# Kernel tuning notes

Hardware: AMD Instinct MI355X
Metric: run time of the kernel (lower is better)

## Reference

```python
import jax, jax.numpy as jnp
import numpy as np

N, E, B, D, L = 100000, 600000, 128, 128, 3
BOT = 64
EPS = 1e-5


def _forward(query_x, corpus_x, gin_eps, mlp_W1, mlp_b1, mlp_W2, mlp_b2, bn_gamma, bn_beta,
             pool_G1, pool_g1b, pool_G2, pool_g2b, pool_Wm,
             int_G1, int_g1b, int_G2, int_g2b, int_F1, int_f1b, int_F2, int_f2b,
             sc_G1, sc_g1b, sc_G2, sc_g2b, sc_F1, sc_f1b, sc_F2, sc_f2b,
             query_edge_index, query_graph_idx, corpus_edge_index, corpus_graph_idx, num_graphs):
    def gin(x, ei, l):
        # GINConv: sum of source-node features into targets, plus (1+eps)*self
        agg = jax.ops.segment_sum(x[ei[0]], ei[1], num_segments=x.shape[0])
        h = (1.0 + gin_eps[l]) * x + agg
        h = jax.nn.relu(h @ mlp_W1[l] + mlp_b1[l]) @ mlp_W2[l] + mlp_b2[l]
        mu = h.mean(axis=0)
        var = ((h - mu) ** 2).mean(axis=0)  # biased var (BatchNorm training mode)
        h = (h - mu) * jax.lax.rsqrt(var + EPS) * bn_gamma[l] + bn_beta[l]
        return jax.nn.relu(h)  # dropout p=0.0

    def pool(x, gidx, l):
        coef = jnp.tanh(jax.nn.relu(x @ pool_G1[l] + pool_g1b[l]) @ pool_G2[l] + pool_g2b[l])
        s = (coef + 1.0) * x
        sums = jax.ops.segment_sum(s, gidx, num_segments=num_graphs)
        cnt = jax.ops.segment_sum(jnp.ones((x.shape[0],), x.dtype), gidx, num_segments=num_graphs)
        mean = sums / cnt[:, None]
        gc = jnp.tanh(mean @ pool_Wm[l])  # [B, D]
        node_coef = jax.nn.sigmoid(jnp.sum(s * gc[gidx], axis=1))  # [N]
        return jax.ops.segment_sum(node_coef[:, None] * s, gidx, num_segments=num_graphs)

    def interact(q, c, l):
        comb = jnp.concatenate([q, c], axis=1)  # [B, 2D]
        coef = jax.nn.sigmoid(jax.nn.relu(comb @ int_G1[l] + int_g1b[l]) @ int_G2[l] + int_g2b[l])
        sc = (coef + 1.0) * comb
        return jax.nn.relu(jax.nn.relu(sc @ int_F1[l] + int_f1b[l]) @ int_F2[l] + int_f2b[l])

    qx, cx = query_x, corpus_x
    feats = []
    for l in range(gin_eps.shape[0]):
        qx = gin(qx, query_edge_index, l)
        cx = gin(cx, corpus_edge_index, l)
        feats.append(interact(pool(qx, query_graph_idx, l), pool(cx, corpus_graph_idx, l), l))
    f = jnp.concatenate(feats, axis=1)  # [B, sum(filters)//2]
    coef = jax.nn.sigmoid(jax.nn.relu(f @ sc_G1 + sc_g1b) @ sc_G2 + sc_g2b)
    sf = (coef + 1.0) * f
    return (jax.nn.relu(sf @ sc_F1 + sc_f1b) @ sc_F2 + sc_f2b).squeeze(-1)  # [B]


def setup_inputs() -> dict:
    key = jax.random.key(0)
    kit = iter(jax.random.split(key, 64))
    def nrm(shape, s=0.05):
        return jax.random.normal(next(kit), shape, jnp.float32) * s
    C, R, OUT, AGG, RG = 2 * D, (2 * D) // 4, D // 2, (3 * D) // 2, ((3 * D) // 2) // 4
    inp = {
        "query_x": nrm((N, D), 1.0),
        "query_edge_index": jax.random.randint(next(kit), (2, E), 0, N),
        "query_graph_idx": jnp.sort(jax.random.randint(next(kit), (N,), 0, B)),
        "corpus_x": nrm((N, D), 1.0),
        "corpus_edge_index": jax.random.randint(next(kit), (2, E), 0, N),
        "corpus_graph_idx": jnp.sort(jax.random.randint(next(kit), (N,), 0, B)),
        "num_graphs": B,
        "gin_eps": jnp.zeros((L,), jnp.float32),
        "mlp_W1": nrm((L, D, D)), "mlp_b1": jnp.zeros((L, D)),
        "mlp_W2": nrm((L, D, D)), "mlp_b2": jnp.zeros((L, D)),
        "bn_gamma": jnp.ones((L, D)), "bn_beta": jnp.zeros((L, D)),
        "pool_G1": nrm((L, D, D // 4)), "pool_g1b": jnp.zeros((L, D // 4)),
        "pool_G2": nrm((L, D // 4, D)), "pool_g2b": jnp.zeros((L, D)),
        "pool_Wm": nrm((L, D, D)),
        "int_G1": nrm((L, C, R)), "int_g1b": jnp.zeros((L, R)),
        "int_G2": nrm((L, R, C)), "int_g2b": jnp.zeros((L, C)),
        "int_F1": nrm((L, C, C)), "int_f1b": jnp.zeros((L, C)),
        "int_F2": nrm((L, C, OUT)), "int_f2b": jnp.zeros((L, OUT)),
        "sc_G1": nrm((AGG, RG)), "sc_g1b": jnp.zeros((RG,)),
        "sc_G2": nrm((RG, AGG)), "sc_g2b": jnp.zeros((AGG,)),
        "sc_F1": nrm((AGG, BOT)), "sc_f1b": jnp.zeros((BOT,)),
        "sc_F2": nrm((BOT, 1)), "sc_f2b": jnp.zeros((1,)),
    }
    return inp


def reference(query_x, query_edge_index, query_graph_idx, corpus_x, corpus_edge_index, corpus_graph_idx,
              num_graphs, gin_eps, mlp_W1, mlp_b1, mlp_W2, mlp_b2, bn_gamma, bn_beta,
              pool_G1, pool_g1b, pool_G2, pool_g2b, pool_Wm,
              int_G1, int_g1b, int_G2, int_g2b, int_F1, int_f1b, int_F2, int_f2b,
              sc_G1, sc_g1b, sc_G2, sc_g2b, sc_F1, sc_f1b, sc_F2, sc_f2b):
    return _forward(query_x, corpus_x, gin_eps, mlp_W1, mlp_b1, mlp_W2, mlp_b2, bn_gamma, bn_beta,
                    pool_G1, pool_g1b, pool_G2, pool_g2b, pool_Wm,
                    int_G1, int_g1b, int_G2, int_g2b, int_F1, int_f1b, int_F2, int_f2b,
                    sc_G1, sc_g1b, sc_G2, sc_g2b, sc_F1, sc_f1b, sc_F2, sc_f2b,
                    query_edge_index, query_graph_idx, corpus_edge_index, corpus_graph_idx, num_graphs)
```

## Files before the change

### kernel.cpp

```cpp
#include <hip/hip_runtime.h>
#include <hip/hip_bf16.h>

constexpr int NN  = 100000;
constexpr int NN2 = 200000;
constexpr int NE  = 600000;
constexpr int NB  = 128;
constexpr int D   = 128;
constexpr int NL  = 3;
constexpr int CAP = 48;
constexpr int MT_TOT = NN2 / 16;
constexpr int MT_Q   = NN / 16;

constexpr int PREP_CSR   = (2 * NE + 255) / 256;
constexpr int PREP_WPREP = 1956;
constexpr int PREP_CNT   = 64;
constexpr int PREP_TOT   = PREP_CSR + PREP_WPREP + PREP_CNT;

constexpr int NCSEG_BLK = 1024;

typedef __bf16 bf16x8 __attribute__((ext_vector_type(8)));
typedef float f32x4 __attribute__((ext_vector_type(4)));
typedef unsigned short us8 __attribute__((ext_vector_type(8)));

__device__ __forceinline__ float sigmoidf_(float x) { return 1.0f / (1.0f + __expf(-x)); }
__device__ __forceinline__ unsigned short f2b(float f) {
    __hip_bfloat16 h = __float2bfloat16(f);
    return __builtin_bit_cast(unsigned short, h);
}
__device__ __forceinline__ float b2f(unsigned short u) {
    __hip_bfloat16 h = __builtin_bit_cast(__hip_bfloat16, u);
    return __bfloat162float(h);
}
__device__ __forceinline__ bf16x8 ldfrag(const unsigned short* p) {
    return __builtin_bit_cast(bf16x8, *(const us8*)p);
}

__device__ __forceinline__ void ncseg_body(int vbid, int nstream_blocks,
                                           const unsigned short* __restrict__ S,
                                           const int* __restrict__ gq, const int* __restrict__ gc,
                                           const float* __restrict__ gcb,
                                           float* __restrict__ dq, float* __restrict__ dc) {
    int stream = vbid * 4 + (threadIdx.x >> 6);
    int lane = threadIdx.x & 63;
    int nstream = nstream_blocks * 4;
    int per = (NN2 + nstream - 1) / nstream;
    int r0 = stream * per;
    int r1 = min(r0 + per, NN2);
    if (r0 >= r1) return;
    float a0 = 0.f, a1 = 0.f;
    int cur = (r0 < NN) ? gq[r0] : 128 + gc[r0 - NN];
    for (int r = r0; r < r1; ++r) {
        int g = (r < NN) ? gq[r] : 128 + gc[r - NN];
        if (g != cur) {
            float* base = (cur < 128) ? (dq + cur * D) : (dc + (cur - 128) * D);
            atomicAdd(&base[lane * 2], a0);
            atomicAdd(&base[lane * 2 + 1], a1);
            a0 = 0.f; a1 = 0.f; cur = g;
        }
        ushort2 sv = *(const ushort2*)&S[(size_t)r * D + lane * 2];
        float2 gv = *(const float2*)&gcb[(size_t)g * D + lane * 2];
        float v0 = b2f(sv.x), v1 = b2f(sv.y);
        float p = v0 * gv.x + v1 * gv.y;
#pragma unroll
        for (int off = 1; off < 64; off <<= 1) p += __shfl_xor(p, off, 64);
        float nc = sigmoidf_(p);
        a0 += nc * v0; a1 += nc * v1;
    }
    float* base = (cur < 128) ? (dq + cur * D) : (dc + (cur - 128) * D);
    atomicAdd(&base[lane * 2], a0);
    atomicAdd(&base[lane * 2 + 1], a1);
}

__device__ __forceinline__ void gather_bf16_body(int vbid,
                                                 const unsigned short* __restrict__ xb,
                                                 unsigned short* __restrict__ z,
                                                 const int* __restrict__ deg, const int* __restrict__ bucket,
                                                 float e) {
    int r = vbid * 16 + (threadIdx.x >> 4);
    int c8 = threadIdx.x & 15;
    float a[8];
    us8 v = *(const us8*)(xb + (size_t)r * D + c8 * 8);
#pragma unroll
    for (int j = 0; j < 8; ++j) a[j] = e * b2f(v[j]);
    int d = deg[r]; d = (d < CAP) ? d : CAP;
    const int* bk = bucket + (size_t)r * CAP;
    int i = 0;
    for (; i + 4 <= d; i += 4) {
        int s0 = bk[i], s1 = bk[i + 1], s2 = bk[i + 2], s3 = bk[i + 3];
        us8 u0 = *(const us8*)(xb + (size_t)s0 * D + c8 * 8);
        us8 u1 = *(const us8*)(xb + (size_t)s1 * D + c8 * 8);
        us8 u2 = *(const us8*)(xb + (size_t)s2 * D + c8 * 8);
        us8 u3 = *(const us8*)(xb + (size_t)s3 * D + c8 * 8);
#pragma unroll
        for (int j = 0; j < 8; ++j)
            a[j] += b2f(u0[j]) + b2f(u1[j]) + b2f(u2[j]) + b2f(u3[j]);
    }
    for (; i < d; ++i) {
        int s0 = bk[i];
        us8 u0 = *(const us8*)(xb + (size_t)s0 * D + c8 * 8);
#pragma unroll
        for (int j = 0; j < 8; ++j) a[j] += b2f(u0[j]);
    }
    us8 o;
#pragma unroll
    for (int j = 0; j < 8; ++j) o[j] = f2b(a[j]);
    *(us8*)(z + (size_t)r * D + c8 * 8) = o;
}

__global__ __launch_bounds__(256) void k_prep(
    const int* __restrict__ qei, const int* __restrict__ cei,
    int* __restrict__ deg, int* __restrict__ bucket,
    const float* mW1, const float* mW2, const float* pG1, const float* pG2,
    const float* iG1, const float* iG2, const float* iF1, const float* iF2,
    const float* sG1, const float* sG2, const float* sF1,
    unsigned short* W1t, unsigned short* W2t, unsigned short* G1t, unsigned short* G2t,
    unsigned short* iG1t, unsigned short* iG2t, unsigned short* iF1t, unsigned short* iF2t,
    unsigned short* sG1t, unsigned short* sG2t, unsigned short* sF1t,
    const int* __restrict__ gq, const int* __restrict__ gc, float* __restrict__ cnt) {
    if (blockIdx.x < PREP_CSR) {
        int e = blockIdx.x * 256 + threadIdx.x;
        int src, dst;
        if (e < NE) {
            src = qei[e]; dst = qei[NE + e];
        } else if (e < 2 * NE) {
            src = cei[e - NE] + NN; dst = cei[NE + (e - NE)] + NN;
        } else return;
        int pos = atomicAdd(&deg[dst], 1);
        if (pos < CAP) bucket[(size_t)dst * CAP + pos] = src;
        return;
    }
    if (blockIdx.x < PREP_CSR + PREP_WPREP) {
        int i = (blockIdx.x - PREP_CSR) * 256 + threadIdx.x;
#define SEG(CNT, KK, NN_, SRC, DST)                                              \
        if (i < (CNT)) {                                                         \
            int l = i / ((KK) * (NN_)), r = i % ((KK) * (NN_));                  \
            int n = r / (KK), k = r % (KK);                                      \
            DST[i] = f2b(SRC[(size_t)l * (KK) * (NN_) + (size_t)k * (NN_) + n]); \
            return;                                                              \
        }                                                                        \
        i -= (CNT);
        SEG(49152, 128, 128, mW1, W1t)
        SEG(49152, 128, 128, mW2, W2t)
        SEG(12288, 128, 32, pG1, G1t)
        SEG(12288, 32, 128, pG2, G2t)
        SEG(49152, 256, 64, iG1, iG1t)
        SEG(49152, 64, 256, iG2, iG2t)
        SEG(196608, 256, 256, iF1, iF1t)
        SEG(49152, 256, 64, iF2, iF2t)
        SEG(9216, 192, 48, sG1, sG1t)
        if (i < 12288) {
            int n = i / 64, k = i % 64;
            sG2t[i] = (k < 48) ? f2b(sG2[(size_t)k * 192 + n]) : (unsigned short)0;
            return;
        }
        i -= 12288;
        SEG(12288, 192, 64, sF1, sF1t)
#undef SEG
        return;
    }
    {
        __shared__ float h[256];
        int vb = blockIdx.x - (PREP_CSR + PREP_WPREP);
        for (int i = threadIdx.x; i < 256; i += 256) h[i] = 0.f;
        __syncthreads();
        int total = PREP_CNT * 256;
        int tid = vb * 256 + threadIdx.x;
        int per = (NN2 + total - 1) / total;
        int r0 = tid * per, r1 = min(r0 + per, NN2);
        if (r0 < r1) {
            int cur = (r0 < NN) ? gq[r0] : 128 + gc[r0 - NN];
            float c = 0.f;
            for (int r = r0; r < r1; ++r) {
                int g = (r < NN) ? gq[r] : 128 + gc[r - NN];
                if (g != cur) { atomicAdd(&h[cur], c); c = 0.f; cur = g; }
                c += 1.f;
            }
            atomicAdd(&h[cur], c);
        }
        __syncthreads();
        for (int i = threadIdx.x; i < 256; i += 256)
            if (h[i] != 0.f) atomicAdd(&cnt[i], h[i]);
    }
}

__global__ __launch_bounds__(256) void k_gather0(const float* __restrict__ qx, const float* __restrict__ cx,
                                                 unsigned short* __restrict__ z,
                                                 const int* __restrict__ deg, const int* __restrict__ bucket,
                                                 const float* __restrict__ eps_p) {
    int r = blockIdx.x * 16 + (threadIdx.x >> 4);
    int c8 = threadIdx.x & 15;
    float e = 1.0f + eps_p[0];
    float a[8];
    const float* base = (r < NN) ? qx : cx;
    int off = (r < NN) ? 0 : NN;
    float4 v0 = *(const float4*)(base + (size_t)(r - off) * D + c8 * 8);
    float4 v1 = *(const float4*)(base + (size_t)(r - off) * D + c8 * 8 + 4);
    a[0] = e * v0.x; a[1] = e * v0.y; a[2] = e * v0.z; a[3] = e * v0.w;
    a[4] = e * v1.x; a[5] = e * v1.y; a[6] = e * v1.z; a[7] = e * v1.w;
    int d = deg[r]; d = (d < CAP) ? d : CAP;
    const int* bk = bucket + (size_t)r * CAP;
    int i = 0;
    for (; i + 4 <= d; i += 4) {
        int s0 = bk[i], s1 = bk[i + 1], s2 = bk[i + 2], s3 = bk[i + 3];
        const float* p0 = base + (size_t)(s0 - off) * D + c8 * 8;
        const float* p1 = base + (size_t)(s1 - off) * D + c8 * 8;
        const float* p2 = base + (size_t)(s2 - off) * D + c8 * 8;
        const float* p3 = base + (size_t)(s3 - off) * D + c8 * 8;
        float4 w0 = *(const float4*)p0, w0b = *(const float4*)(p0 + 4);
        float4 w1 = *(const float4*)p1, w1b = *(const float4*)(p1 + 4);
        float4 w2 = *(const float4*)p2, w2b = *(const float4*)(p2 + 4);
        float4 w3 = *(const float4*)p3, w3b = *(const float4*)(p3 + 4);
        a[0] += w0.x + w1.x + w2.x + w3.x; a[1] += w0.y + w1.y + w2.y + w3.y;
        a[2] += w0.z + w1.z + w2.z + w3.z; a[3] += w0.w + w1.w + w2.w + w3.w;
        a[4] += w0b.x + w1b.x + w2b.x + w3b.x; a[5] += w0b.y + w1b.y + w2b.y + w3b.y;
        a[6] += w0b.z + w1b.z + w2b.z + w3b.z; a[7] += w0b.w + w1b.w + w2b.w + w3b.w;
    }
    for (; i < d; ++i) {
        int s0 = bk[i];
        const float* p0 = base + (size_t)(s0 - off) * D + c8 * 8;
        float4 w0 = *(const float4*)p0, w0b = *(const float4*)(p0 + 4);
        a[0] += w0.x; a[1] += w0.y; a[2] += w0.z; a[3] += w0.w;
        a[4] += w0b.x; a[5] += w0b.y; a[6] += w0b.z; a[7] += w0b.w;
    }
    us8 o;
#pragma unroll
    for (int j = 0; j < 8; ++j) o[j] = f2b(a[j]);
    *(us8*)(z + (size_t)r * D + c8 * 8) = o;
}

__global__ __launch_bounds__(256) void k_gncseg(const unsigned short* __restrict__ xb,
                                                unsigned short* __restrict__ z,
                                                const int* __restrict__ deg, const int* __restrict__ bucket,
                                                const float* __restrict__ eps_p, int l,
                                                const unsigned short* __restrict__ S,
                                                const int* __restrict__ gq, const int* __restrict__ gcix,
                                                const float* __restrict__ gcb,
                                                float* __restrict__ dq, float* __restrict__ dc) {
    if (blockIdx.x < NCSEG_BLK) {
        ncseg_body(blockIdx.x, NCSEG_BLK, S, gq, gcix, gcb, dq, dc);
    } else {
        float e = 1.0f + eps_p[l];
        gather_bf16_body(blockIdx.x - NCSEG_BLK, xb, z, deg, bucket, e);
    }
}

__global__ __launch_bounds__(256) void k_ncseg(const unsigned short* __restrict__ S,
                                               const int* __restrict__ gq, const int* __restrict__ gc,
                                               const float* __restrict__ gcb,
                                               float* __restrict__ dq, float* __restrict__ dc) {
    ncseg_body(blockIdx.x, NCSEG_BLK, S, gq, gc, gcb, dq, dc);
}

constexpr int HSTR = 136;
__global__ __launch_bounds__(256, 2) void k_mlp(unsigned short* zh,
                                                const unsigned short* __restrict__ W1t,
                                                const unsigned short* __restrict__ W2t,
                                                const float* __restrict__ b1,
                                                const float* __restrict__ b2,
                                                float* __restrict__ stat) {
    __shared__ unsigned short hb[2][2][16 * HSTR];
    __shared__ float red[512];
    int wave = threadIdx.x >> 6, lane = threadIdx.x & 63;
    int col16 = lane & 15, quad = lane >> 4;
    int g = wave >> 1, half = wave & 1;
    bf16x8 bf1[4][4], bf2[4][4];
    float bb1[4], bb2[4];
#pragma unroll
    for (int t = 0; t < 4; ++t) {
        int c = half * 64 + t * 16 + col16;
        bb1[t] = b1[c]; bb2[t] = b2[c];
#pragma unroll
        for (int kc = 0; kc < 4; ++kc) {
            bf1[t][kc] = ldfrag(W1t + (size_t)c * D + kc * 32 + quad * 8);
            bf2[t][kc] = ldfrag(W2t + (size_t)c * D + kc * 32 + quad * 8);
        }
    }
    float cs[2][4] = {{0.f,0.f,0.f,0.f},{0.f,0.f,0.f,0.f}};
    float cq[2][4] = {{0.f,0.f,0.f,0.f},{0.f,0.f,0.f,0.f}};
    int groups = gridDim.x * 2;
    int iters = (MT_TOT + groups - 1) / groups;
    for (int n = 0; n < iters; ++n) {
        int mt = blockIdx.x * 2 + g + n * groups;
        bool act = (mt < MT_TOT);
        int pp = n & 1;
        unsigned short* hbuf = hb[pp][g];
        {
            const unsigned short* Ap = zh + ((size_t)(act ? mt : 0) * 16 + col16) * D + quad * 8;
            f32x4 acc[4];
#pragma unroll
            for (int t = 0; t < 4; ++t) acc[t] = (f32x4){0.f, 0.f, 0.f, 0.f};
#pragma unroll
            for (int kc = 0; kc < 4; ++kc) {
                bf16x8 af = ldfrag(Ap + kc * 32);
#pragma unroll
                for (int t = 0; t < 4; ++t)
                    acc[t] = __builtin_amdgcn_mfma_f32_16x16x32_bf16(af, bf1[t][kc], acc[t], 0, 0, 0);
            }
#pragma unroll
            for (int t = 0; t < 4; ++t) {
                int c = half * 64 + t * 16 + col16;
#pragma unroll
                for (int r = 0; r < 4; ++r)
                    hbuf[(quad * 4 + r) * HSTR + c] = f2b(fmaxf(acc[t][r] + bb1[t], 0.f));
            }
        }
        __syncthreads();
        {
            f32x4 acc[4];
#pragma unroll
            for (int t = 0; t < 4; ++t) acc[t] = (f32x4){0.f, 0.f, 0.f, 0.f};
#pragma unroll
            for (int kc = 0; kc < 4; ++kc) {
                bf16x8 af = ldfrag(&hbuf[col16 * HSTR + kc * 32 + quad * 8]);
#pragma unroll
                for (int t = 0; t < 4; ++t)
                    acc[t] = __builtin_amdgcn_mfma_f32_16x16x32_bf16(af, bf2[t][kc], acc[t], 0, 0, 0);
            }
            if (act) {
                int side = (mt < MT_Q) ? 0 : 1;
#pragma unroll
                for (int t = 0; t < 4; ++t) {
                    int c = half * 64 + t * 16 + col16;
#pragma unroll
                    for (int r = 0; r < 4; ++r) {
                        int m = mt * 16 + quad * 4 + r;
                        float v = acc[t][r] + bb2[t];
                        zh[(size_t)m * D + c] = f2b(v);
                        cs[side][t] += v; cq[side][t] += v * v;
                    }
                }
            }
        }
    }
    for (int i = threadIdx.x; i < 512; i += 256) red[i] = 0.f;
    __syncthreads();
#pragma unroll
    for (int t = 0; t < 4; ++t) {
        int c = half * 64 + t * 16 + col16;
#pragma unroll
        for (int side = 0; side < 2; ++side) {
            atomicAdd(&red[side * 256 + c], cs[side][t]);
            atomicAdd(&red[side * 256 + 128 + c], cq[side][t]);
        }
    }
    __syncthreads();
    for (int i = threadIdx.x; i < 512; i += 256) atomicAdd(&stat[i], red[i]);
}

__global__ __launch_bounds__(256, 2) void k_pool(const unsigned short* __restrict__ H,
                                                 const unsigned short* __restrict__ G1t,
                                                 const unsigned short* __restrict__ G2t,
                                                 const float* __restrict__ b1,
                                                 const float* __restrict__ b2,
                                                 const float* __restrict__ stat,
                                                 const float* __restrict__ gamma,
                                                 const float* __restrict__ beta,
                                                 const int* __restrict__ gq, const int* __restrict__ gcix,
                                                 unsigned short* __restrict__ Xo,
                                                 unsigned short* __restrict__ S,
                                                 float* __restrict__ seg_sum) {
    __shared__ float sc_s[256], sh_s[256];
    __shared__ unsigned short xt[4][16 * HSTR];
    __shared__ unsigned short t2t[4][16 * 40];
    {
        int t = threadIdx.x, side = t >> 7, c = t & 127;
        const float invN = 1.0f / (float)NN;
        float mu = stat[side * 256 + c] * invN;
        float var = fmaxf(stat[side * 256 + 128 + c] * invN - mu * mu, 0.f);
        float inv = rsqrtf(var + 1e-5f);
        float s = gamma[c] * inv;
        sc_s[t] = s;
        sh_s[t] = beta[c] - mu * s;
    }
    __syncthreads();
    int wave = threadIdx.x >> 6, lane = threadIdx.x & 63;
    int col16 = lane & 15, quad = lane >> 4;
    unsigned short* xtile = xt[wave];
    unsigned short* t2tile = t2t[wave];
    int nwaves = gridDim.x * 4;
    int per = (MT_TOT + nwaves - 1) / nwaves;
    int wid = blockIdx.x * 4 + wave;
    int mt0 = wid * per, mt1 = min(mt0 + per, MT_TOT);
    if (mt0 >= mt1) return;

    bf16x8 g1f[2][4], g2f[8];
    float bb1[2], bb2[8];
#pragma unroll
    for (int t = 0; t < 2; ++t) {
        int c = t * 16 + col16;
        bb1[t] = b1[c];
#pragma unroll
        for (int kc = 0; kc < 4; ++kc)
            g1f[t][kc] = ldfrag(G1t + (size_t)c * D + kc * 32 + quad * 8);
    }
#pragma unroll
    for (int t = 0; t < 8; ++t) {
        int c = t * 16 + col16;
        bb2[t] = b2[c];
        g2f[t] = ldfrag(G2t + (size_t)c * 32 + quad * 8);
    }
    float sacc[8] = {0.f, 0.f, 0.f, 0.f, 0.f, 0.f, 0.f, 0.f};
    int curg = -1;
    for (int mt = mt0; mt < mt1; ++mt) {
        int side = (mt < MT_Q) ? 0 : 1;
        const float* scp = sc_s + side * 128;
        const float* shp = sh_s + side * 128;
        const unsigned short* Hp = H + ((size_t)mt * 16 + col16) * D + quad * 8;
        unsigned short* Xp = Xo + ((size_t)mt * 16 + col16) * D + quad * 8;
        f32x4 acc1[2];
#pragma unroll
        for (int t = 0; t < 2; ++t) acc1[t] = (f32x4){0.f, 0.f, 0.f, 0.f};
#pragma unroll
        for (int kc = 0; kc < 4; ++kc) {
            us8 hv = *(const us8*)(Hp + kc * 32);
            int k0 = kc * 32 + quad * 8;
            float4 s0 = *(const float4*)&scp[k0], s1 = *(const float4*)&scp[k0 + 4];
            float4 h0 = *(const float4*)&shp[k0], h1 = *(const float4*)&shp[k0 + 4];
            us8 xv;
            xv[0] = f2b(fmaxf(b2f(hv[0]) * s0.x + h0.x, 0.f));
            xv[1] = f2b(fmaxf(b2f(hv[1]) * s0.y + h0.y, 0.f));
            xv[2] = f2b(fmaxf(b2f(hv[2]) * s0.z + h0.z, 0.f));
            xv[3] = f2b(fmaxf(b2f(hv[3]) * s0.w + h0.w, 0.f));
            xv[4] = f2b(fmaxf(b2f(hv[4]) * s1.x + h1.x, 0.f));
            xv[5] = f2b(fmaxf(b2f(hv[5]) * s1.y + h1.y, 0.f));
            xv[6] = f2b(fmaxf(b2f(hv[6]) * s1.z + h1.z, 0.f));
            xv[7] = f2b(fmaxf(b2f(hv[7]) * s1.w + h1.w, 0.f));
            *(us8*)(Xp + kc * 32) = xv;
            *(us8*)(xtile + col16 * HSTR + k0) = xv;
            bf16x8 af = __builtin_bit_cast(bf16x8, xv);
#pragma unroll
            for (int t = 0; t < 2; ++t)
                acc1[t] = __builtin_amdgcn_mfma_f32_16x16x32_bf16(af, g1f[t][kc], acc1[t], 0, 0, 0);
        }
#pragma unroll
        for (int t = 0; t < 2; ++t) {
            int c = t * 16 + col16;
#pragma unroll
            for (int r = 0; r < 4; ++r)
                t2tile[(quad * 4 + r) * 40 + c] = f2b(fmaxf(acc1[t][r] + bb1[t], 0.f));
        }
        bf16x8 af2 = ldfrag(t2tile + col16 * 40 + quad * 8);
        f32x4 acc2[8];
#pragma unroll
        for (int t = 0; t < 8; ++t) {
            acc2[t] = (f32x4){0.f, 0.f, 0.f, 0.f};
            acc2[t] = __builtin_amdgcn_mfma_f32_16x16x32_bf16(af2, g2f[t], acc2[t], 0, 0, 0);
        }
#pragma unroll
        for (int r = 0; r < 4; ++r) {
            int m = mt * 16 + quad * 4 + r;
            int g = (m < NN) ? gq[m] : 128 + gcix[m - NN];
            if (g != curg) {
                if (curg >= 0) {
#pragma unroll
                    for (int t = 0; t < 8; ++t) {
                        atomicAdd(&seg_sum[(size_t)curg * D + t * 16 + col16], sacc[t]);
                        sacc[t] = 0.f;
                    }
                }
                curg = g;
            }
#pragma unroll
            for (int t = 0; t < 8; ++t) {
                int c = t * 16 + col16;
                float v = (tanhf(acc2[t][r] + bb2[t]) + 1.f) * b2f(xtile[(quad * 4 + r) * HSTR + c]);
                S[(size_t)m * D + c] = f2b(v);
                sacc[t] += v;
            }
        }
    }
    if (curg >= 0) {
#pragma unroll
        for (int t = 0; t < 8; ++t)
            atomicAdd(&seg_sum[(size_t)curg * D + t * 16 + col16], sacc[t]);
    }
}

__global__ void k_gc(float* __restrict__ sums, const float* __restrict__ cnt,
                     const float* __restrict__ Wm, float* __restrict__ gc) {
    __shared__ float m[D];
    int b = blockIdx.x, j = threadIdx.x;
    m[j] = sums[b * D + j] / cnt[b];
    sums[b * D + j] = 0.f;
    __syncthreads();
    float a = 0.f;
#pragma unroll 8
    for (int i = 0; i < D; ++i) a += m[i] * Wm[i * D + j];
    gc[b * D + j] = tanhf(a);
}

constexpr int LSTR = 264;
__global__ __launch_bounds__(256) void k_interact(const float* __restrict__ pooled,
                                                  const unsigned short* __restrict__ iG1t, const float* __restrict__ ig1b,
                                                  const unsigned short* __restrict__ iG2t, const float* __restrict__ ig2b,
                                                  const unsigned short* __restrict__ iF1t, const float* __restrict__ if1b,
                                                  const unsigned short* __restrict__ iF2t, const float* __restrict__ if2b,
                                                  unsigned short* __restrict__ featsb) {
    __shared__ unsigned short bufC[16 * LSTR];
    __shared__ unsigned short bufA[16 * LSTR];
    __shared__ unsigned short bufB[16 * LSTR];
    int t = threadIdx.x, wave = t >> 6, lane = t & 63;
    int col16 = lane & 15, quad = lane >> 4;
    int pg = blockIdx.x & 7, l = blockIdx.x >> 3;
    int p0 = pg * 16;
    {
        int r = t >> 4, c0 = (t & 15) * 16;
        const float* src = (c0 < 128)
            ? (pooled + (size_t)l * NB * D + (size_t)(p0 + r) * D + c0)
            : (pooled + (size_t)(NL + l) * NB * D + (size_t)(p0 + r) * D + (c0 - 128));
#pragma unroll
        for (int j = 0; j < 16; ++j) bufC[r * LSTR + c0 + j] = f2b(src[j]);
    }
    __syncthreads();
    {
        f32x4 acc = (f32x4){0.f, 0.f, 0.f, 0.f};
        int n = wave * 16 + col16;
#pragma unroll
        for (int kc = 0; kc < 8; ++kc) {
            bf16x8 af = ldfrag(&bufC[col16 * LSTR + kc * 32 + quad * 8]);
            bf16x8 bfr = ldfrag(iG1t + ((size_t)l * 64 + n) * 256 + kc * 32 + quad * 8);
            acc = __builtin_amdgcn_mfma_f32_16x16x32_bf16(af, bfr, acc, 0, 0, 0);
        }
        float bb = ig1b[(size_t)l * 64 + n];
#pragma unroll
        for (int r = 0; r < 4; ++r)
            bufA[(quad * 4 + r) * LSTR + n] = f2b(fmaxf(acc[r] + bb, 0.f));
    }
    __syncthreads();
    {
        f32x4 acc[4];
#pragma unroll
        for (int tt = 0; tt < 4; ++tt) acc[tt] = (f32x4){0.f, 0.f, 0.f, 0.f};
#pragma unroll
        for (int kc = 0; kc < 2; ++kc) {
            bf16x8 af = ldfrag(&bufA[col16 * LSTR + kc * 32 + quad * 8]);
#pragma unroll
            for (int tt = 0; tt < 4; ++tt) {
                int n = wave * 64 + tt * 16 + col16;
                bf16x8 bfr = ldfrag(iG2t + ((size_t)l * 256 + n) * 64 + kc * 32 + quad * 8);
                acc[tt] = __builtin_amdgcn_mfma_f32_16x16x32_bf16(af, bfr, acc[tt], 0, 0, 0);
            }
        }
#pragma unroll
        for (int tt = 0; tt < 4; ++tt) {
            int n = wave * 64 + tt * 16 + col16;
            float bb = ig2b[(size_t)l * 256 + n];
#pragma unroll
            for (int r = 0; r < 4; ++r) {
                int row = quad * 4 + r;
                float s = (sigmoidf_(acc[tt][r] + bb) + 1.f) * b2f(bufC[row * LSTR + n]);
                bufB[row * LSTR + n] = f2b(s);
            }
        }
    }
    __syncthreads();
    {
        f32x4 acc[4];
#pragma unroll
        for (int tt = 0; tt < 4; ++tt) acc[tt] = (f32x4){0.f, 0.f, 0.f, 0.f};
#pragma unroll
        for (int kc = 0; kc < 8; ++kc) {
            bf16x8 af = ldfrag(&bufB[col16 * LSTR + kc * 32 + quad * 8]);
#pragma unroll
            for (int tt = 0; tt < 4; ++tt) {
                int n = wave * 64 + tt * 16 + col16;
                bf16x8 bfr = ldfrag(iF1t + (size_t)l * 256 * 256 + (size_t)n * 256 + kc * 32 + quad * 8);
                acc[tt] = __builtin_amdgcn_mfma_f32_16x16x32_bf16(af, bfr, acc[tt], 0, 0, 0);
            }
        }
#pragma unroll
        for (int tt = 0; tt < 4; ++tt) {
            int n = wave * 64 + tt * 16 + col16;
            float bb = if1b[(size_t)l * 256 + n];
#pragma unroll
            for (int r = 0; r < 4; ++r)
                bufA[(quad * 4 + r) * LSTR + n] = f2b(fmaxf(acc[tt][r] + bb, 0.f));
        }
    }
    __syncthreads();
    {
        f32x4 acc = (f32x4){0.f, 0.f, 0.f, 0.f};
        int n = wave * 16 + col16;
#pragma unroll
        for (int kc = 0; kc < 8; ++kc) {
            bf16x8 af = ldfrag(&bufA[col16 * LSTR + kc * 32 + quad * 8]);
            bf16x8 bfr = ldfrag(iF2t + ((size_t)l * 64 + n) * 256 + kc * 32 + quad * 8);
            acc = __builtin_amdgcn_mfma_f32_16x16x32_bf16(af, bfr, acc, 0, 0, 0);
        }
        float bb = if2b[(size_t)l * 64 + n];
#pragma unroll
        for (int r = 0; r < 4; ++r)
            featsb[(size_t)(p0 + quad * 4 + r) * 192 + l * 64 + n] = f2b(fmaxf(acc[r] + bb, 0.f));
    }
}

__global__ __launch_bounds__(256) void k_score(const unsigned short* __restrict__ featsb,
                                               const unsigned short* __restrict__ sG1t, const float* __restrict__ sg1b,
                                               const unsigned short* __restrict__ sG2t, const float* __restrict__ sg2b,
                                               const unsigned short* __restrict__ sF1t, const float* __restrict__ sf1b,
                                               const float* __restrict__ sF2, const float* __restrict__ sf2b,
                                               float* __restrict__ out) {
    __shared__ unsigned short bufF[16 * 200];
    __shared__ unsigned short bufA[16 * LSTR];
    __shared__ unsigned short bufB[16 * LSTR];
    __shared__ float redf[16 * 65];
    int t = threadIdx.x, wave = t >> 6, lane = t & 63;
    int col16 = lane & 15, quad = lane >> 4;
    int p0 = blockIdx.x * 16;
    {
        int r = t >> 4, c0 = (t & 15) * 12;
#pragma unroll
        for (int j = 0; j < 12; ++j)
            bufF[r * 200 + c0 + j] = featsb[(size_t)(p0 + r) * 192 + c0 + j];
    }
    __syncthreads();
    if (wave < 3) {
        f32x4 acc = (f32x4){0.f, 0.f, 0.f, 0.f};
        int n = wave * 16 + col16;
#pragma unroll
        for (int kc = 0; kc < 6; ++kc) {
            bf16x8 af = ldfrag(&bufF[col16 * 200 + kc * 32 + quad * 8]);
            bf16x8 bfr = ldfrag(sG1t + (size_t)n * 192 + kc * 32 + quad * 8);
            acc = __builtin_amdgcn_mfma_f32_16x16x32_bf16(af, bfr, acc, 0, 0, 0);
        }
        float bb = sg1b[n];
#pragma unroll
        for (int r = 0; r < 4; ++r)
            bufA[(quad * 4 + r) * LSTR + n] = f2b(fmaxf(acc[r] + bb, 0.f));
    } else {
        int row = lane >> 2, c = 48 + (lane & 3) * 4;
#pragma unroll
        for (int j = 0; j < 4; ++j) bufA[row * LSTR + c + j] = 0;
    }
    __syncthreads();
    {
        f32x4 acc[3];
#pragma unroll
        for (int tt = 0; tt < 3; ++tt) acc[tt] = (f32x4){0.f, 0.f, 0.f, 0.f};
#pragma unroll
        for (int kc = 0; kc < 2; ++kc) {
            bf16x8 af = ldfrag(&bufA[col16 * LSTR + kc * 32 + quad * 8]);
#pragma unroll
            for (int tt = 0; tt < 3; ++tt) {
                int n = wave * 48 + tt * 16 + col16;
                bf16x8 bfr = ldfrag(sG2t + (size_t)n * 64 + kc * 32 + quad * 8);
                acc[tt] = __builtin_amdgcn_mfma_f32_16x16x32_bf16(af, bfr, acc[tt], 0, 0, 0);
            }
        }
#pragma unroll
        for (int tt = 0; tt < 3; ++tt) {
            int n = wave * 48 + tt * 16 + col16;
            float bb = sg2b[n];
#pragma unroll
            for (int r = 0; r < 4; ++r) {
                int row = quad * 4 + r;
                float s = (sigmoidf_(acc[tt][r] + bb) + 1.f) * b2f(bufF[row * 200 + n]);
                bufB[row * LSTR + n] = f2b(s);
            }
        }
    }
    __syncthreads();
    {
        f32x4 acc = (f32x4){0.f, 0.f, 0.f, 0.f};
        int n = wave * 16 + col16;
#pragma unroll
        for (int kc = 0; kc < 6; ++kc) {
            bf16x8 af = ldfrag(&bufB[col16 * LSTR + kc * 32 + quad * 8]);
            bf16x8 bfr = ldfrag(sF1t + (size_t)n * 192 + kc * 32 + quad * 8);
            acc = __builtin_amdgcn_mfma_f32_16x16x32_bf16(af, bfr, acc, 0, 0, 0);
        }
        float bb = sf1b[n], w2 = sF2[n];
#pragma unroll
        for (int r = 0; r < 4; ++r)
            redf[(quad * 4 + r) * 65 + n] = fmaxf(acc[r] + bb, 0.f) * w2;
    }
    __syncthreads();
    if (t < 16) {
        float s = 0.f;
#pragma unroll 8
        for (int i = 0; i < 64; ++i) s += redf[t * 65 + i];
        out[p0 + t] = s + sf2b[0];
    }
}

extern "C" void kernel_launch(void* const* d_in, const int* in_sizes, int n_in,
                              void* d_out, int out_size, void* d_ws, size_t ws_size,
                              hipStream_t stream) {
    const float* query_x   = (const float*)d_in[0];
    const int*   query_ei  = (const int*)d_in[1];
    const int*   query_gi  = (const int*)d_in[2];
    const float* corpus_x  = (const float*)d_in[3];
    const int*   corpus_ei = (const int*)d_in[4];
    const int*   corpus_gi = (const int*)d_in[5];
    const float* gin_eps   = (const float*)d_in[7];
    const float* mlp_W1    = (const float*)d_in[8];
    const float* mlp_b1    = (const float*)d_in[9];
    const float* mlp_W2    = (const float*)d_in[10];
    const float* mlp_b2    = (const float*)d_in[11];
    const float* bn_gamma  = (const float*)d_in[12];
    const float* bn_beta   = (const float*)d_in[13];
    const float* pool_G1   = (const float*)d_in[14];
    const float* pool_g1b  = (const float*)d_in[15];
    const float* pool_G2   = (const float*)d_in[16];
    const float* pool_g2b  = (const float*)d_in[17];
    const float* pool_Wm   = (const float*)d_in[18];
    const float* int_G1    = (const float*)d_in[19];
    const float* int_g1b   = (const float*)d_in[20];
    const float* int_G2    = (const float*)d_in[21];
    const float* int_g2b   = (const float*)d_in[22];
    const float* int_F1    = (const float*)d_in[23];
    const float* int_f1b   = (const float*)d_in[24];
    const float* int_F2    = (const float*)d_in[25];
    const float* int_f2b   = (const float*)d_in[26];
    const float* sc_G1     = (const float*)d_in[27];
    const float* sc_g1b    = (const float*)d_in[28];
    const float* sc_G2     = (const float*)d_in[29];
    const float* sc_g2b    = (const float*)d_in[30];
    const float* sc_F1     = (const float*)d_in[31];
    const float* sc_f1b    = (const float*)d_in[32];
    const float* sc_F2     = (const float*)d_in[33];
    const float* sc_f2b    = (const float*)d_in[34];
    float* out = (float*)d_out;

    unsigned short* Zb  = (unsigned short*)d_ws;
    unsigned short* Xb  = Zb + (size_t)NN2 * D;
    unsigned short* Sb  = Xb + (size_t)NN2 * D;
    unsigned short* featsb = Sb + (size_t)NN2 * D;
    unsigned short* W1t = featsb + 128 * 192;
    unsigned short* W2t = W1t + NL * D * D;
    unsigned short* G1t = W2t + NL * D * D;
    unsigned short* G2t = G1t + NL * 32 * D;
    unsigned short* iG1t = G2t + NL * D * 32;
    unsigned short* iG2t = iG1t + NL * 64 * 256;
    unsigned short* iF1t = iG2t + NL * 256 * 64;
    unsigned short* iF2t = iF1t + NL * 256 * 256;
    unsigned short* sG1t = iF2t + NL * 64 * 256;
    unsigned short* sG2t = sG1t + 48 * 192;
    unsigned short* sF1t = sG2t + 192 * 64;
    int* deg    = (int*)(sF1t + 64 * 192);
    int* bucket = deg + NN2;
    float* bn_stat  = (float*)(bucket + (size_t)NN2 * CAP);
    float* seg_sum  = bn_stat + NL * 512;
    float* seg_cnt  = seg_sum + 256 * D;
    float* gcb      = seg_cnt + 256;
    float* pooled   = gcb + 256 * D;

    hipMemsetAsync(deg, 0, NN2 * sizeof(int), stream);
    hipMemsetAsync(bn_stat, 0, NL * 512 * sizeof(float), stream);
    hipMemsetAsync(pooled, 0, 2 * NL * NB * D * sizeof(float), stream);
    hipMemsetAsync(seg_cnt, 0, 256 * sizeof(float), stream);
    hipMemsetAsync(seg_sum, 0, 256 * D * sizeof(float), stream);

    k_prep<<<PREP_TOT, 256, 0, stream>>>(query_ei, corpus_ei, deg, bucket,
                                         mlp_W1, mlp_W2, pool_G1, pool_G2,
                                         int_G1, int_G2, int_F1, int_F2,
                                         sc_G1, sc_G2, sc_F1,
                                         W1t, W2t, G1t, G2t, iG1t, iG2t, iF1t, iF2t,
                                         sG1t, sG2t, sF1t,
                                         query_gi, corpus_gi, seg_cnt);

    for (int l = 0; l < NL; ++l) {
        if (l == 0)
            k_gather0<<<MT_TOT, 256, 0, stream>>>(query_x, corpus_x, Zb, deg, bucket, gin_eps);
        else
            k_gncseg<<<NCSEG_BLK + MT_TOT, 256, 0, stream>>>(
                Xb, Zb, deg, bucket, gin_eps, l,
                Sb, query_gi, corpus_gi, gcb,
                pooled + (size_t)(l - 1) * NB * D,
                pooled + (size_t)(NL + l - 1) * NB * D);
        k_mlp<<<1024, 256, 0, stream>>>(Zb, W1t + (size_t)l * D * D, W2t + (size_t)l * D * D,
                                        mlp_b1 + l * D, mlp_b2 + l * D, bn_stat + l * 512);
        k_pool<<<782, 256, 0, stream>>>(Zb, G1t + (size_t)l * 32 * D, G2t + (size_t)l * D * 32,
                                        pool_g1b + l * 32, pool_g2b + l * D,
                                        bn_stat + l * 512, bn_gamma + l * D, bn_beta + l * D,
                                        query_gi, corpus_gi, Xb, Sb, seg_sum);
        k_gc<<<256, D, 0, stream>>>(seg_sum, seg_cnt, pool_Wm + (size_t)l * D * D, gcb);
    }
    k_ncseg<<<NCSEG_BLK, 256, 0, stream>>>(Sb, query_gi, corpus_gi, gcb,
                                           pooled + (size_t)(NL - 1) * NB * D,
                                           pooled + (size_t)(2 * NL - 1) * NB * D);
    k_interact<<<24, 256, 0, stream>>>(pooled, iG1t, int_g1b, iG2t, int_g2b,
                                       iF1t, int_f1b, iF2t, int_f2b, featsb);
    k_score<<<8, 256, 0, stream>>>(featsb, sG1t, sc_g1b, sG2t, sc_g2b,
                                   sF1t, sc_f1b, sc_F2, sc_f2b, out);
}
```

Measured before the change: 998.4 us.

## Restructure MLP kernel to one 32-row tile per block, stream weights from cache

The MLP kernel moves from a persistent grid, where each wave kept its 64-column weight slice in registers, to one block per 32-row tile. Each wave computes 32 columns for both 16-row halves and reloads the W1/W2 fragments from global memory or cache. The block reduces BatchNorm statistics in LDS and adds them to global memory once per block. In the pool kernel, the G1/G2 weight fragments are likewise loaded per tile instead of kept in registers, and the occupancy hints go up (4 and 3 blocks per CU). The goal is to cut register pressure and raise occupancy, in exchange for repeated weight loads and many more global atomics on the stats.

After: 1.227 ms. 22.9% more time.

```diff
diff --git a/kernel.cpp b/kernel.cpp
--- a/kernel.cpp
+++ b/kernel.cpp
@@ -10,6 +10,7 @@
 constexpr int CAP = 48;
 constexpr int MT_TOT = NN2 / 16;
 constexpr int MT_Q   = NN / 16;
+constexpr int ST_TOT = NN2 / 32;
 
 constexpr int PREP_CSR   = (2 * NE + 255) / 256;
 constexpr int PREP_WPREP = 1956;
@@ -252,102 +253,91 @@
 }
 
 constexpr int HSTR = 136;
-__global__ __launch_bounds__(256, 2) void k_mlp(unsigned short* zh,
+__global__ __launch_bounds__(256, 4) void k_mlp(unsigned short* zh,
                                                 const unsigned short* __restrict__ W1t,
                                                 const unsigned short* __restrict__ W2t,
                                                 const float* __restrict__ b1,
                                                 const float* __restrict__ b2,
                                                 float* __restrict__ stat) {
-    __shared__ unsigned short hb[2][2][16 * HSTR];
-    __shared__ float red[512];
-    int wave = threadIdx.x >> 6, lane = threadIdx.x & 63;
+    __shared__ unsigned short hbuf[32 * HSTR];
+    __shared__ float red[256];
+    int tid = threadIdx.x;
+    int wave = tid >> 6, lane = tid & 63;
     int col16 = lane & 15, quad = lane >> 4;
-    int g = wave >> 1, half = wave & 1;
-    bf16x8 bf1[4][4], bf2[4][4];
-    float bb1[4], bb2[4];
-#pragma unroll
-    for (int t = 0; t < 4; ++t) {
-        int c = half * 64 + t * 16 + col16;
-        bb1[t] = b1[c]; bb2[t] = b2[c];
+    int base = blockIdx.x * 32;
+    red[tid] = 0.f;
+    {
+        f32x4 acc[2][2];
+#pragma unroll
+        for (int rt = 0; rt < 2; ++rt)
+#pragma unroll
+            for (int ct = 0; ct < 2; ++ct) acc[rt][ct] = (f32x4){0.f, 0.f, 0.f, 0.f};
 #pragma unroll
         for (int kc = 0; kc < 4; ++kc) {
-            bf1[t][kc] = ldfrag(W1t + (size_t)c * D + kc * 32 + quad * 8);
-            bf2[t][kc] = ldfrag(W2t + (size_t)c * D + kc * 32 + quad * 8);
-        }
-    }
-    float cs[2][4] = {{0.f,0.f,0.f,0.f},{0.f,0.f,0.f,0.f}};
-    float cq[2][4] = {{0.f,0.f,0.f,0.f},{0.f,0.f,0.f,0.f}};
-    int groups = gridDim.x * 2;
-    int iters = (MT_TOT + groups - 1) / groups;
-    for (int n = 0; n < iters; ++n) {
-        int mt = blockIdx.x * 2 + g + n * groups;
-        bool act = (mt < MT_TOT);
-        int pp = n & 1;
-        unsigned short* hbuf = hb[pp][g];
-        {
-            const unsigned short* Ap = zh + ((size_t)(act ? mt : 0) * 16 + col16) * D + quad * 8;
-            f32x4 acc[4];
-#pragma unroll
-            for (int t = 0; t < 4; ++t) acc[t] = (f32x4){0.f, 0.f, 0.f, 0.f};
-#pragma unroll
-            for (int kc = 0; kc < 4; ++kc) {
-                bf16x8 af = ldfrag(Ap + kc * 32);
-#pragma unroll
-                for (int t = 0; t < 4; ++t)
-                    acc[t] = __builtin_amdgcn_mfma_f32_16x16x32_bf16(af, bf1[t][kc], acc[t], 0, 0, 0);
-            }
-#pragma unroll
-            for (int t = 0; t < 4; ++t) {
-                int c = half * 64 + t * 16 + col16;
+            bf16x8 af0 = ldfrag(zh + (size_t)(base + col16) * D + kc * 32 + quad * 8);
+            bf16x8 af1 = ldfrag(zh + (size_t)(base + 16 + col16) * D + kc * 32 + quad * 8);
+#pragma unroll
+            for (int ct = 0; ct < 2; ++ct) {
+                int c = wave * 32 + ct * 16 + col16;
+                bf16x8 wf = ldfrag(W1t + (size_t)c * D + kc * 32 + quad * 8);
+                acc[0][ct] = __builtin_amdgcn_mfma_f32_16x16x32_bf16(af0, wf, acc[0][ct], 0, 0, 0);
+                acc[1][ct] = __builtin_amdgcn_mfma_f32_16x16x32_bf16(af1, wf, acc[1][ct], 0, 0, 0);
+            }
+        }
+#pragma unroll
+        for (int ct = 0; ct < 2; ++ct) {
+            int c = wave * 32 + ct * 16 + col16;
+            float bb = b1[c];
+#pragma unroll
+            for (int rt = 0; rt < 2; ++rt)
 #pragma unroll
                 for (int r = 0; r < 4; ++r)
-                    hbuf[(quad * 4 + r) * HSTR + c] = f2b(fmaxf(acc[t][r] + bb1[t], 0.f));
-            }
+                    hbuf[(rt * 16 + quad * 4 + r) * HSTR + c] = f2b(fmaxf(acc[rt][ct][r] + bb, 0.f));
+        }
+    }
+    __syncthreads();
+    {
+        f32x4 acc[2][2];
+#pragma unroll
+        for (int rt = 0; rt < 2; ++rt)
+#pragma unroll
+            for (int ct = 0; ct < 2; ++ct) acc[rt][ct] = (f32x4){0.f, 0.f, 0.f, 0.f};
+#pragma unroll
+        for (int kc = 0; kc < 4; ++kc) {
+            bf16x8 af0 = ldfrag(hbuf + col16 * HSTR + kc * 32 + quad * 8);
+            bf16x8 af1 = ldfrag(hbuf + (16 + col16) * HSTR + kc * 32 + quad * 8);
+#pragma unroll
+            for (int ct = 0; ct < 2; ++ct) {
+                int c = wave * 32 + ct * 16 + col16;
+                bf16x8 wf = ldfrag(W2t + (size_t)c * D + kc * 32 + quad * 8);
+                acc[0][ct] = __builtin_amdgcn_mfma_f32_16x16x32_bf16(af0, wf, acc[0][ct], 0, 0, 0);
+                acc[1][ct] = __builtin_amdgcn_mfma_f32_16x16x32_bf16(af1, wf, acc[1][ct], 0, 0, 0);
+            }
+        }
+        int side = (base < NN) ? 0 : 1;
+#pragma unroll
+        for (int ct = 0; ct < 2; ++ct) {
+            int c = wave * 32 + ct * 16 + col16;
+            float bb = b2[c];
+            float ssum = 0.f, ssq = 0.f;
+#pragma unroll
+            for (int rt = 0; rt < 2; ++rt)
+#pragma unroll
+                for (int r = 0; r < 4; ++r) {
+                    int m = base + rt * 16 + quad * 4 + r;
+                    float v = acc[rt][ct][r] + bb;
+                    zh[(size_t)m * D + c] = f2b(v);
+                    ssum += v; ssq += v * v;
+                }
+            atomicAdd(&red[c], ssum);
+            atomicAdd(&red[128 + c], ssq);
         }
         __syncthreads();
-        {
-            f32x4 acc[4];
-#pragma unroll
-            for (int t = 0; t < 4; ++t) acc[t] = (f32x4){0.f, 0.f, 0.f, 0.f};
-#pragma unroll
-            for (int kc = 0; kc < 4; ++kc) {
-                bf16x8 af = ldfrag(&hbuf[col16 * HSTR + kc * 32 + quad * 8]);
-#pragma unroll
-                for (int t = 0; t < 4; ++t)
-                    acc[t] = __builtin_amdgcn_mfma_f32_16x16x32_bf16(af, bf2[t][kc], acc[t], 0, 0, 0);
-            }
-            if (act) {
-                int side = (mt < MT_Q) ? 0 : 1;
-#pragma unroll
-                for (int t = 0; t < 4; ++t) {
-                    int c = half * 64 + t * 16 + col16;
-#pragma unroll
-                    for (int r = 0; r < 4; ++r) {
-                        int m = mt * 16 + quad * 4 + r;
-                        float v = acc[t][r] + bb2[t];
-                        zh[(size_t)m * D + c] = f2b(v);
-                        cs[side][t] += v; cq[side][t] += v * v;
-                    }
-                }
-            }
-        }
-    }
-    for (int i = threadIdx.x; i < 512; i += 256) red[i] = 0.f;
-    __syncthreads();
-#pragma unroll
-    for (int t = 0; t < 4; ++t) {
-        int c = half * 64 + t * 16 + col16;
-#pragma unroll
-        for (int side = 0; side < 2; ++side) {
-            atomicAdd(&red[side * 256 + c], cs[side][t]);
-            atomicAdd(&red[side * 256 + 128 + c], cq[side][t]);
-        }
-    }
-    __syncthreads();
-    for (int i = threadIdx.x; i < 512; i += 256) atomicAdd(&stat[i], red[i]);
-}
-
-__global__ __launch_bounds__(256, 2) void k_pool(const unsigned short* __restrict__ H,
+        atomicAdd(&stat[side * 256 + tid], red[tid]);
+    }
+}
+
+__global__ __launch_bounds__(256, 3) void k_pool(const unsigned short* __restrict__ H,
                                                  const unsigned short* __restrict__ G1t,
                                                  const unsigned short* __restrict__ G2t,
                                                  const float* __restrict__ b1,
@@ -383,22 +373,11 @@
     int mt0 = wid * per, mt1 = min(mt0 + per, MT_TOT);
     if (mt0 >= mt1) return;
 
-    bf16x8 g1f[2][4], g2f[8];
     float bb1[2], bb2[8];
 #pragma unroll
-    for (int t = 0; t < 2; ++t) {
-        int c = t * 16 + col16;
-        bb1[t] = b1[c];
-#pragma unroll
-        for (int kc = 0; kc < 4; ++kc)
-            g1f[t][kc] = ldfrag(G1t + (size_t)c * D + kc * 32 + quad * 8);
-    }
-#pragma unroll
-    for (int t = 0; t < 8; ++t) {
-        int c = t * 16 + col16;
-        bb2[t] = b2[c];
-        g2f[t] = ldfrag(G2t + (size_t)c * 32 + quad * 8);
-    }
+    for (int t = 0; t < 2; ++t) bb1[t] = b1[t * 16 + col16];
+#pragma unroll
+    for (int t = 0; t < 8; ++t) bb2[t] = b2[t * 16 + col16];
     float sacc[8] = {0.f, 0.f, 0.f, 0.f, 0.f, 0.f, 0.f, 0.f};
     int curg = -1;
     for (int mt = mt0; mt < mt1; ++mt) {
@@ -429,8 +408,10 @@
             *(us8*)(xtile + col16 * HSTR + k0) = xv;
             bf16x8 af = __builtin_bit_cast(bf16x8, xv);
 #pragma unroll
-            for (int t = 0; t < 2; ++t)
-                acc1[t] = __builtin_amdgcn_mfma_f32_16x16x32_bf16(af, g1f[t][kc], acc1[t], 0, 0, 0);
+            for (int t = 0; t < 2; ++t) {
+                bf16x8 wf = ldfrag(G1t + (size_t)(t * 16 + col16) * D + kc * 32 + quad * 8);
+                acc1[t] = __builtin_amdgcn_mfma_f32_16x16x32_bf16(af, wf, acc1[t], 0, 0, 0);
+            }
         }
 #pragma unroll
         for (int t = 0; t < 2; ++t) {
@@ -443,8 +424,9 @@
         f32x4 acc2[8];
 #pragma unroll
         for (int t = 0; t < 8; ++t) {
+            bf16x8 wf = ldfrag(G2t + (size_t)(t * 16 + col16) * 32 + quad * 8);
             acc2[t] = (f32x4){0.f, 0.f, 0.f, 0.f};
-            acc2[t] = __builtin_amdgcn_mfma_f32_16x16x32_bf16(af2, g2f[t], acc2[t], 0, 0, 0);
+            acc2[t] = __builtin_amdgcn_mfma_f32_16x16x32_bf16(af2, wf, acc2[t], 0, 0, 0);
         }
 #pragma unroll
         for (int r = 0; r < 4; ++r) {
@@ -768,8 +750,8 @@
                 Sb, query_gi, corpus_gi, gcb,
                 pooled + (size_t)(l - 1) * NB * D,
                 pooled + (size_t)(NL + l - 1) * NB * D);
-        k_mlp<<<1024, 256, 0, stream>>>(Zb, W1t + (size_t)l * D * D, W2t + (size_t)l * D * D,
-                                        mlp_b1 + l * D, mlp_b2 + l * D, bn_stat + l * 512);
+        k_mlp<<<ST_TOT, 256, 0, stream>>>(Zb, W1t + (size_t)l * D * D, W2t + (size_t)l * D * D,
+                                          mlp_b1 + l * D, mlp_b2 + l * D, bn_stat + l * 512);
         k_pool<<<782, 256, 0, stream>>>(Zb, G1t + (size_t)l * 32 * D, G2t + (size_t)l * D * 32,
                                         pool_g1b + l * 32, pool_g2b + l * D,
                                         bn_stat + l * 512, bn_gamma + l * D, bn_beta + l * D,
```
